# Performance work log

Hardware: AMD Instinct MI355X
Metric: run time of the kernel (lower is better)

The kernel has to match this reference:

```python
import jax, jax.numpy as jnp
import numpy as np

N_EMBD = 1024
N_HEADS = 16
HEAD_DIM = N_EMBD // N_HEADS  # 64
NUM_BUCKETS = 32
MAX_DISTANCE = 64


def _relative_position_bucket(relative_position):
    # bidirectional=False path from the torch source
    rp = jnp.maximum(-relative_position, 0)  # valid (non-positive) rel positions -> distance
    max_exact = NUM_BUCKETS // 2
    is_small = rp < max_exact
    rp_f = jnp.maximum(rp, 1).astype(jnp.float32)  # guard log(0); masked by where
    large = max_exact + (
        jnp.log(rp_f / max_exact) / np.log(MAX_DISTANCE / max_exact) * (NUM_BUCKETS - max_exact)
    ).astype(jnp.int32)
    large = jnp.minimum(large, NUM_BUCKETS - 1)
    return jnp.where(is_small, rp, large)


def setup_inputs() -> dict:
    key = jax.random.key(0)
    ks = jax.random.split(key, 10)
    B, S = 2, 2048
    std = 1.0 / np.sqrt(N_EMBD)
    inp = {
        "hidden_states": jax.random.normal(ks[0], (B, S, N_EMBD), dtype=jnp.float32),
        "Wq": jax.random.normal(ks[1], (N_EMBD, N_EMBD), dtype=jnp.float32) * std,
        "bq": jnp.zeros((N_EMBD,), jnp.float32),
        "Wk": jax.random.normal(ks[2], (N_EMBD, N_EMBD), dtype=jnp.float32) * std,
        "bk": jnp.zeros((N_EMBD,), jnp.float32),
        "Wv": jax.random.normal(ks[3], (N_EMBD, N_EMBD), dtype=jnp.float32) * std,
        "bv": jnp.zeros((N_EMBD,), jnp.float32),
        "Wo": jax.random.normal(ks[4], (N_EMBD, N_EMBD), dtype=jnp.float32) * std,
        "bo": jnp.zeros((N_EMBD,), jnp.float32),
        "rel_bias": jax.random.normal(ks[5], (NUM_BUCKETS, N_HEADS), dtype=jnp.float32) * 0.1,
    }
    return inp


def reference(hidden_states, Wq, bq, Wk, bk, Wv, bv, Wo, bo, rel_bias):
    B, S, _ = hidden_states.shape

    def shape(x):  # [B,S,E] -> [B,H,S,D]
        return x.reshape(B, S, N_HEADS, HEAD_DIM).transpose(0, 2, 1, 3)

    scale = 1.0 / np.sqrt(HEAD_DIM)
    q = shape(hidden_states @ Wq + bq)
    k = shape(hidden_states @ Wk + bk)
    v = shape(hidden_states @ Wv + bv)

    scores = jnp.einsum("bhqd,bhkd->bhqk", q * scale, k)

    ctx = jnp.arange(S)[:, None]
    mem = jnp.arange(S)[None, :]
    bucket = _relative_position_bucket(mem - ctx)  # [S,S] int
    # [S,S,H] -> [1,H,S,S]
    position_bias = rel_bias[bucket].transpose(2, 0, 1)[None]
    scores = scores + position_bias * 8.0  # note the *8 from the source

    attn = jax.nn.softmax(scores.astype(jnp.float32), axis=-1).astype(scores.dtype)
    ctx_out = jnp.einsum("bhqk,bhkd->bhqd", attn, v)
    ctx_out = ctx_out.transpose(0, 2, 1, 3).reshape(B, S, N_EMBD)
    return ctx_out @ Wo + bo
```

## Files before the change

### kernel.cpp

```cpp
#include <hip/hip_runtime.h>
#include <math.h>


#define SEQ 2048
#define EMB 1024
#define NH 16
#define HD 64
#define LOG2E 1.44269504088896340736f
#define MU (1u << 20)

typedef short v8s __attribute__((ext_vector_type(8)));
typedef float v4f __attribute__((ext_vector_type(4)));
typedef float v16f __attribute__((ext_vector_type(16)));
typedef unsigned int v4u __attribute__((ext_vector_type(4)));

__device__ __forceinline__ v4f mfma16(v8s a, v8s b, v4f c) {
  return __builtin_amdgcn_mfma_f32_16x16x32_bf16(a, b, c, 0, 0, 0);
}
__device__ __forceinline__ v16f mfma32(v8s a, v8s b, v16f c) {
  return __builtin_amdgcn_mfma_f32_32x32x16_bf16(a, b, c, 0, 0, 0);
}
__device__ __forceinline__ unsigned short bfh(float x) {
  unsigned u = __builtin_bit_cast(unsigned, x);
  return (unsigned short)((u + 0x7FFFu + ((u >> 16) & 1u)) >> 16);
}
__device__ __forceinline__ float bff(unsigned short h) {
  unsigned u = (unsigned)h << 16;
  return __builtin_bit_cast(float, u);
}
__device__ __forceinline__ int imin(int a, int b) { return a < b ? a : b; }
__device__ __forceinline__ unsigned pk2(float a, float b) {
  unsigned h;
  asm("v_cvt_pk_bf16_f32 %0, %1, %2" : "=v"(h) : "v"(a), "v"(b));
  return h;
}
__device__ __forceinline__ void split2(float a, float b, unsigned& uh, unsigned& ul) {
  const unsigned h = pk2(a, b);
  const float ra = __builtin_bit_cast(float, h << 16);
  const float rb = __builtin_bit_cast(float, h & 0xFFFF0000u);
  uh = h;
  ul = pk2(a - ra, b - rb);
}
typedef const __attribute__((address_space(1))) unsigned char* gp_t;
typedef __attribute__((address_space(3))) unsigned char* lp_t;
__device__ __forceinline__ void gload16(const void* g, void* l) {
  __builtin_amdgcn_global_load_lds((gp_t)g, (lp_t)l, 16, 0, 0);
}

__global__ __launch_bounds__(256) void prep_kernel(
    const float* __restrict__ hs, const float* __restrict__ Wq,
    const float* __restrict__ Wk, const float* __restrict__ Wv,
    const float* __restrict__ Wo, unsigned short* __restrict__ wsu) {
  __shared__ float T[64][68];
  const int t = threadIdx.x;
  const int z = blockIdx.z;
  if (z == 4) {
    unsigned short* ah = wsu + 32u * MU;
    const int base = (blockIdx.y * 16 + blockIdx.x) * 16384 + t * 4;
#pragma unroll
    for (int i = 0; i < 16; ++i) {
      const int idx = base + i * 1024;
      const float4 v = *(const float4*)(hs + idx);
      *(uint2*)&ah[idx] = make_uint2(pk2(v.x, v.y), pk2(v.z, v.w));
    }
    return;
  }
  const float* W = (z == 0) ? Wq : (z == 1) ? Wk : (z == 2) ? Wv : Wo;
  const float s = (z == 0) ? 0.125f * LOG2E : 1.0f;
  unsigned short* WTh = wsu + (size_t)(40u + 2u * z) * MU;
  unsigned short* WTl = WTh + MU;
  const int n0 = blockIdx.x * 64, k0 = blockIdx.y * 64;
  const int r = t >> 2, cs = (t & 3) * 16;
#pragma unroll
  for (int i = 0; i < 4; ++i)
    *(float4*)&T[r][cs + i * 4] =
        *(const float4*)(W + (size_t)(k0 + r) * EMB + n0 + cs + i * 4);
  __syncthreads();
  unsigned short hb[16], lb[16];
#pragma unroll
  for (int i = 0; i < 16; i += 2) {
    unsigned uh, ul;
    split2(T[cs + i][r] * s, T[cs + i + 1][r] * s, uh, ul);
    hb[i] = (unsigned short)(uh & 0xFFFFu);
    hb[i + 1] = (unsigned short)(uh >> 16);
    lb[i] = (unsigned short)(ul & 0xFFFFu);
    lb[i + 1] = (unsigned short)(ul >> 16);
  }
  const size_t go = (size_t)(n0 + r) * EMB + k0 + cs;
  *(v8s*)&WTh[go] = *(v8s*)&hb[0];
  *(v8s*)&WTh[go + 8] = *(v8s*)&hb[8];
  *(v8s*)&WTl[go] = *(v8s*)&lb[0];
  *(v8s*)&WTl[go + 8] = *(v8s*)&lb[8];
}

struct alignas(16) G2Smem {
  unsigned short Ah[128][32], Bh[128][32], Bl[128][32];
};

__device__ __forceinline__ void gemm128_2p(
    const unsigned short* __restrict__ Ah_g,
    const unsigned short* __restrict__ Bh_g,
    const unsigned short* __restrict__ Bl_g,
    int m0, int n0, G2Smem& S, v4f acc[4][4]) {
  const int t = threadIdx.x;
  const int l = t & 63, w = t >> 6;
  const int wm = (w >> 1) << 6, wn = (w & 1) << 6;
  const int lg = l >> 4, lc = l & 15;
  const int r0 = t >> 2;
  const int gl = (t & 3) ^ ((r0 >> 1) & 3);
  unsigned short* lba = &S.Ah[0][0] + w * 512;
  unsigned short* lbb = &S.Bh[0][0] + w * 512;
  unsigned short* lbl = &S.Bl[0][0] + w * 512;
  for (int k0 = 0; k0 < EMB; k0 += 32) {
    __syncthreads();
    {
      const size_t sa0 = (size_t)(m0 + r0) * EMB + k0 + gl * 8;
      const size_t sb0 = (size_t)(n0 + r0) * EMB + k0 + gl * 8;
      gload16(Ah_g + sa0, lba);
      gload16(Ah_g + sa0 + (size_t)64 * EMB, lba + 2048);
      gload16(Bh_g + sb0, lbb);
      gload16(Bh_g + sb0 + (size_t)64 * EMB, lbb + 2048);
      gload16(Bl_g + sb0, lbl);
      gload16(Bl_g + sb0 + (size_t)64 * EMB, lbl + 2048);
    }
    asm volatile("s_waitcnt vmcnt(0)" ::: "memory");
    __syncthreads();
    v8s ah[4], bh[4], bl[4];
#pragma unroll
    for (int r = 0; r < 4; ++r) {
      const int ra = wm + r * 16 + lc;
      ah[r] = *(const v8s*)&S.Ah[ra][(lg ^ ((ra >> 1) & 3)) * 8];
      const int rb = wn + r * 16 + lc;
      bh[r] = *(const v8s*)&S.Bh[rb][(lg ^ ((rb >> 1) & 3)) * 8];
      bl[r] = *(const v8s*)&S.Bl[rb][(lg ^ ((rb >> 1) & 3)) * 8];
    }
#pragma unroll
    for (int i = 0; i < 4; ++i)
#pragma unroll
      for (int j = 0; j < 4; ++j) {
        acc[i][j] = mfma16(ah[i], bh[j], acc[i][j]);
        acc[i][j] = mfma16(ah[i], bl[j], acc[i][j]);
      }
  }
  __syncthreads();
}

__global__ __launch_bounds__(256) void qkv_mfma(
    const float* __restrict__ bq, const float* __restrict__ bk,
    const float* __restrict__ bv, unsigned short* __restrict__ wsu) {
  __shared__ G2Smem S;
  const int mat = blockIdx.y >> 3;
  const int m0 = blockIdx.x << 7, n0 = (blockIdx.y & 7) << 7;
  const unsigned short* Ah_g = wsu + 32u * MU;
  const unsigned short* Bh_g = wsu + (size_t)(40u + 2u * mat) * MU;
  const unsigned short* Bl_g = Bh_g + MU;
  const float* bias = (mat == 0) ? bq : (mat == 1) ? bk : bv;
  const float bs = (mat == 0) ? 0.125f * LOG2E : 1.0f;
  unsigned short* oh = wsu + (size_t)mat * 8u * MU;
  unsigned short* ol = oh + 4u * MU;

  v4f acc[4][4] = {};
  gemm128_2p(Ah_g, Bh_g, Bl_g, m0, n0, S, acc);

  const int t = threadIdx.x, l = t & 63, w = t >> 6;
  const int wm = (w >> 1) << 6, wn = (w & 1) << 6, lg = l >> 4, lc = l & 15;
  if (mat == 0) {
#pragma unroll
    for (int i = 0; i < 4; ++i)
#pragma unroll
      for (int j = 0; j < 4; ++j)
#pragma unroll
        for (int jr = 0; jr < 4; ++jr) {
          const int r = m0 + wm + i * 16 + lg * 4 + jr;
          const int cm = n0 + wn + j * 16 + lc;
          const float val = acc[i][j][jr] + bias[cm] * bs;
          const unsigned short h = bfh(val);
          const size_t idx = (((size_t)((r >> 11) * NH + (cm >> 6)) * SEQ) +
                              (r & 2047)) * HD + (cm & 63);
          oh[idx] = h;
          ol[idx] = bfh(val - bff(h));
        }
  } else if (mat == 1) {
#pragma unroll
    for (int i = 0; i < 4; ++i)
#pragma unroll
      for (int j = 0; j < 4; ++j)
#pragma unroll
        for (int jr = 0; jr < 4; ++jr) {
          const int r = m0 + wm + i * 16 + lg * 4 + jr;
          const int cm = n0 + wn + j * 16 + lc;
          const float val = acc[i][j][jr] + bias[cm];
          const int s = r & 2047, d = cm & 63;
          const size_t idx = (((size_t)((r >> 11) * NH + (cm >> 6)) * SEQ) + s) * HD +
                             ((((d >> 3) ^ (s & 7)) << 3) | (d & 7));
          oh[idx] = bfh(val);
        }
  } else {
    unsigned short* Traw = &S.Ah[0][0];
    unsigned short (*Th)[136] = (unsigned short(*)[136])Traw;
    unsigned short (*Tl)[136] = (unsigned short(*)[136])(Traw + 32 * 136);
    const int b = m0 >> 11;
    const int s0base = m0 & 2047;
#pragma unroll
    for (int j = 0; j < 4; ++j) {
      __syncthreads();
#pragma unroll
      for (int i = 0; i < 4; ++i)
#pragma unroll
        for (int jr = 0; jr < 4; ++jr) {
          const int cm = n0 + wn + j * 16 + lc;
          const float val = acc[i][j][jr] + bias[cm];
          const unsigned short hi = bfh(val);
          const int trow = (wn >> 2) + lc;
          const int tcol = wm + i * 16 + lg * 4 + jr;
          Th[trow][tcol] = hi;
          Tl[trow][tcol] = bfh(val - bff(hi));
        }
      __syncthreads();
      const int tr = t >> 3, sgc = (t & 7) * 16;
      const int c = n0 + (tr >> 4) * 64 + j * 16 + (tr & 15);
      const int h2 = c >> 6, d = c & 63;
      const int sabs = s0base + sgc;
      const int g0 = (sabs >> 3) & 7;
      const size_t ob = ((size_t)(b * NH + h2) * HD + d) * SEQ + (sabs & ~63);
      const int o0 = (g0 ^ (d & 7)) << 3, o1 = ((g0 + 1) ^ (d & 7)) << 3;
      *(v8s*)&oh[ob + o0] = *(const v8s*)&Th[tr][sgc];
      *(v8s*)&oh[ob + o1] = *(const v8s*)&Th[tr][sgc + 8];
      *(v8s*)&ol[ob + o0] = *(const v8s*)&Tl[tr][sgc];
      *(v8s*)&ol[ob + o1] = *(const v8s*)&Tl[tr][sgc + 8];
    }
  }
}

__device__ __forceinline__ v8s pfrag(unsigned a0, unsigned a1, unsigned a2,
                                     unsigned a3, int h5) {
  const unsigned sa = (unsigned)__shfl_xor((int)(h5 ? a0 : a2), 32, 64);
  const unsigned sb = (unsigned)__shfl_xor((int)(h5 ? a1 : a3), 32, 64);
  v4u r;
  r[0] = h5 ? sa : a0;
  r[1] = h5 ? sb : a1;
  r[2] = h5 ? a2 : sa;
  r[3] = h5 ? a3 : sb;
  return __builtin_bit_cast(v8s, r);
}

__global__ __launch_bounds__(256, 3) void attn_mfma(
    const float* __restrict__ rel_bias, unsigned short* __restrict__ wsu) {
  __shared__ struct alignas(16) {
    unsigned short Kh[2][64][64];
    unsigned short VTh[2][64][64];
    unsigned short VTl[2][64][64];
    float bias8[32];
  } S;
  const int t = threadIdx.x;
  const int nid = (blockIdx.x & 7) * 128 + (blockIdx.x >> 3);
  const int half = nid >> 9;
  const int bh = (nid >> 4) & 31;
  const int qt = nid & 15;
  const int hh = bh & 15, b = bh >> 4;
  const int w = t >> 6, l = t & 63;
  const int lq = l & 31, h5 = l >> 5;
  const int qbase = qt * 128 + w * 32;
  const int kvbase = half << 10;

  const unsigned short* qh = wsu;
  const unsigned short* ql = wsu + 4u * MU;
  const unsigned short* kh = wsu + 8u * MU;
  const unsigned short* vth = wsu + 16u * MU;
  const unsigned short* vtl = wsu + 20u * MU;
  unsigned short* od = wsu + (half ? 28u : 24u) * MU;
  float2* stats = (float2*)(wsu + 36u * MU);

  if (t < 32) S.bias8[t] = rel_bias[t * NH + hh] * 8.0f * LOG2E;

  v8s qfh[4], qfl[4];
  const size_t qg = ((size_t)bh * SEQ + qbase + lq) * HD;
#pragma unroll
  for (int dc = 0; dc < 4; ++dc) {
    qfh[dc] = *(const v8s*)(qh + qg + dc * 16 + h5 * 8);
    qfl[dc] = *(const v8s*)(ql + qg + dc * 16 + h5 * 8);
  }

  float m_run = -1e30f, l_run = 0.0f;
  v16f acc[2] = {};

  const int srow = t >> 3, sg = t & 7;
  const size_t kbase_g = ((size_t)bh * SEQ + kvbase) * HD;
  const size_t vbase_g = (size_t)bh * HD * SEQ + kvbase;

  auto stage = [&](int kt, int bufsel) {
    const int kv0 = kt * 64;
    unsigned short* lk = &S.Kh[bufsel][0][0] + w * 512;
    unsigned short* lvh = &S.VTh[bufsel][0][0] + w * 512;
    unsigned short* lvl = &S.VTl[bufsel][0][0] + w * 512;
    gload16(kh + kbase_g + (size_t)(kv0 + srow) * HD + sg * 8, lk);
    gload16(kh + kbase_g + (size_t)(kv0 + srow + 32) * HD + sg * 8, lk + 2048);
    gload16(vth + vbase_g + (size_t)srow * SEQ + kv0 + sg * 8, lvh);
    gload16(vth + vbase_g + (size_t)(srow + 32) * SEQ + kv0 + sg * 8, lvh + 2048);
    gload16(vtl + vbase_g + (size_t)srow * SEQ + kv0 + sg * 8, lvl);
    gload16(vtl + vbase_g + (size_t)(srow + 32) * SEQ + kv0 + sg * 8, lvl + 2048);
  };

  stage(0, 0);
  for (int kt = 0; kt < 16; ++kt) {
    const int buf = kt & 1;
    const int kv0 = kvbase + kt * 64;
    asm volatile("s_waitcnt vmcnt(0)" ::: "memory");
    __syncthreads();
    if (kt < 15) stage(kt + 1, buf ^ 1);

    v16f sc[2] = {};
    __builtin_amdgcn_s_setprio(1);
#pragma unroll
    for (int kb = 0; kb < 2; ++kb)
#pragma unroll
      for (int dc = 0; dc < 4; ++dc) {
        const int cswz = (((dc << 1) + h5) ^ (lq & 7)) << 3;
        const v8s kfh = *(const v8s*)&S.Kh[buf][kb * 32 + lq][cswz];
        sc[kb] = mfma32(kfh, qfh[dc], sc[kb]);
        sc[kb] = mfma32(kfh, qfl[dc], sc[kb]);
      }
    __builtin_amdgcn_s_setprio(0);

#pragma unroll
    for (int kb = 0; kb < 2; ++kb) {
      const int dq = qbase - (kv0 + kb * 32);
      if (dq + 31 <= 0) {
        const float bb = S.bias8[0];
#pragma unroll
        for (int r = 0; r < 16; ++r) sc[kb][r] += bb;
      } else if (dq >= 90) {
        const float bb = S.bias8[31];
#pragma unroll
        for (int r = 0; r < 16; ++r) sc[kb][r] += bb;
      } else {
#pragma unroll
        for (int r = 0; r < 16; ++r) {
          const int krow = (r & 3) + 8 * (r >> 2) + 4 * h5;
          int rp = (qbase + lq) - (kv0 + kb * 32 + krow);
          rp = rp > 0 ? rp : 0;
          const int bu =
              rp < 16 ? rp
                      : imin(16 + (int)(8.0f * __log2f((float)rp * 0.0625f)), 31);
          sc[kb][r] += S.bias8[bu];
        }
      }
    }

    float mt = sc[0][0];
#pragma unroll
    for (int r = 1; r < 16; ++r) mt = fmaxf(mt, sc[0][r]);
#pragma unroll
    for (int r = 0; r < 16; ++r) mt = fmaxf(mt, sc[1][r]);
    mt = fmaxf(mt, __shfl_xor(mt, 32, 64));
    if (__all(mt <= m_run + 8.0f) == 0) {
      const float mn = fmaxf(m_run, mt);
      const float fac = exp2f(m_run - mn);
      l_run *= fac;
#pragma unroll
      for (int r = 0; r < 16; ++r) {
        acc[0][r] *= fac;
        acc[1][r] *= fac;
      }
      m_run = mn;
    }
    unsigned pk[16];
    float rs = 0.0f;
#pragma unroll
    for (int i = 0; i < 16; ++i) {
      const float p0 = exp2f(sc[i >> 3][(2 * i) & 15] - m_run);
      const float p1 = exp2f(sc[i >> 3][(2 * i + 1) & 15] - m_run);
      rs += p0 + p1;
      pk[i] = pk2(p0, p1);
    }
    rs += __shfl_xor(rs, 32, 64);
    l_run += rs;

    __builtin_amdgcn_s_setprio(1);
#pragma unroll
    for (int ks = 0; ks < 4; ++ks) {
      const v8s pb = pfrag(pk[4 * ks], pk[4 * ks + 1], pk[4 * ks + 2],
                           pk[4 * ks + 3], h5);
      const int cswz = (((ks << 1) + h5) ^ (lq & 7)) << 3;
#pragma unroll
      for (int db = 0; db < 2; ++db) {
        const v8s vfh = *(const v8s*)&S.VTh[buf][db * 32 + lq][cswz];
        const v8s vfl = *(const v8s*)&S.VTl[buf][db * 32 + lq][cswz];
        acc[db] = mfma32(vfh, pb, acc[db]);
        acc[db] = mfma32(vfl, pb, acc[db]);
      }
    }
    __builtin_amdgcn_s_setprio(0);
  }

  const float inv = 1.0f / l_run;
  const size_t rowb = ((size_t)b * SEQ + qbase + lq) * EMB + hh * HD;
#pragma unroll
  for (int db = 0; db < 2; ++db)
#pragma unroll
    for (int i = 0; i < 8; ++i) {
      const unsigned u = pk2(acc[db][2 * i] * inv, acc[db][2 * i + 1] * inv);
      const int d0 = db * 32 + 8 * (i >> 1) + 4 * h5 + 2 * (i & 1);
      *(unsigned*)&od[rowb + d0] = u;
    }
  if (h5 == 0)
    stats[(size_t)((half << 5) + bh) * SEQ + qbase + lq] =
        make_float2(m_run, l_run);
}

__global__ __launch_bounds__(256) void merge_kernel(unsigned short* __restrict__ wsu) {
  const int t = threadIdx.x;
  const size_t idx = ((size_t)blockIdx.x * 256 + t) * 16;
  const int row = (int)(idx >> 10);
  const int col = (int)(idx & 1023);
  const int b = row >> 11, s = row & 2047;
  const int bh = b * NH + (col >> 6);
  const float2* st = (const float2*)(wsu + 36u * MU);
  const float2 s0 = st[(size_t)bh * SEQ + s];
  const float2 s1 = st[(size_t)32 * SEQ + (size_t)bh * SEQ + s];
  const float M = fmaxf(s0.x, s1.x);
  const float w0 = s0.y * exp2f(s0.x - M);
  const float w1 = s1.y * exp2f(s1.x - M);
  const float inv = 1.0f / (w0 + w1);
  const float a0 = w0 * inv, a1 = w1 * inv;
  unsigned short* p0 = wsu + 24u * MU + idx;
  const unsigned short* p1 = wsu + 28u * MU + idx;
  const v8s x0a = *(const v8s*)p0, x0b = *(const v8s*)(p0 + 8);
  const v8s x1a = *(const v8s*)p1, x1b = *(const v8s*)(p1 + 8);
  unsigned short o[16];
#pragma unroll
  for (int e = 0; e < 8; ++e) {
    o[e] = bfh(a0 * bff((unsigned short)x0a[e]) + a1 * bff((unsigned short)x1a[e]));
    o[8 + e] =
        bfh(a0 * bff((unsigned short)x0b[e]) + a1 * bff((unsigned short)x1b[e]));
  }
  *(v8s*)p0 = *(const v8s*)&o[0];
  *(v8s*)(p0 + 8) = *(const v8s*)&o[8];
}

__global__ __launch_bounds__(256) void out_mfma(
    const float* __restrict__ bo, float* __restrict__ out,
    unsigned short* __restrict__ wsu) {
  __shared__ G2Smem S;
  const int m0 = blockIdx.x << 7, n0 = blockIdx.y << 7;
  const unsigned short* Ah_g = wsu + 24u * MU;
  const unsigned short* Bh_g = wsu + 46u * MU;
  const unsigned short* Bl_g = wsu + 47u * MU;
  v4f acc[4][4] = {};
  gemm128_2p(Ah_g, Bh_g, Bl_g, m0, n0, S, acc);
  const int t = threadIdx.x, l = t & 63, w = t >> 6;
  const int wm = (w >> 1) << 6, wn = (w & 1) << 6, lg = l >> 4, lc = l & 15;
#pragma unroll
  for (int i = 0; i < 4; ++i)
#pragma unroll
    for (int j = 0; j < 4; ++j)
#pragma unroll
      for (int jr = 0; jr < 4; ++jr) {
        const int r = m0 + wm + i * 16 + lg * 4 + jr;
        const int c = n0 + wn + j * 16 + lc;
        out[(size_t)r * EMB + c] = acc[i][j][jr] + bo[c];
      }
}

extern "C" void kernel_launch(void* const* d_in, const int* in_sizes, int n_in,
                              void* d_out, int out_size, void* d_ws, size_t ws_size,
                              hipStream_t stream) {
  const float* hs = (const float*)d_in[0];
  const float* Wq = (const float*)d_in[1];
  const float* bq = (const float*)d_in[2];
  const float* Wk = (const float*)d_in[3];
  const float* bk = (const float*)d_in[4];
  const float* Wv = (const float*)d_in[5];
  const float* bv = (const float*)d_in[6];
  const float* Wo = (const float*)d_in[7];
  const float* bo = (const float*)d_in[8];
  const float* rb = (const float*)d_in[9];
  unsigned short* wsu = (unsigned short*)d_ws;

  hipLaunchKernelGGL(prep_kernel, dim3(16, 16, 5), dim3(256), 0, stream,
                     hs, Wq, Wk, Wv, Wo, wsu);
  hipLaunchKernelGGL(qkv_mfma, dim3(32, 24), dim3(256), 0, stream, bq, bk, bv, wsu);
  hipLaunchKernelGGL(attn_mfma, dim3(1024), dim3(256), 0, stream, rb, wsu);
  hipLaunchKernelGGL(merge_kernel, dim3(1024), dim3(256), 0, stream, wsu);
  hipLaunchKernelGGL(out_mfma, dim3(32, 8), dim3(256), 0, stream, bo, (float*)d_out, wsu);
}
```

Baseline: 298.6 us.

## Drop low-order bf16 split for K and V paths, change LDS swizzle key

Stops producing and consuming the low-part bf16 correction for Wk, Wv and the V tensor. The K/V projections and the PV matmul now use a single bf16 MFMA instead of two, and less data is loaded into LDS. The freed LDS allows the attention kernel's launch bounds to target 4 blocks per CU instead of 3. The K/V swizzle key is also changed to a new skey function to reduce LDS bank conflicts. In exchange, precision drops on the K/V and PV paths, which may push error past tolerance.

```diff
diff --git a/kernel.cpp b/kernel.cpp
--- a/kernel.cpp
+++ b/kernel.cpp
@@ -45,6 +45,9 @@
 typedef __attribute__((address_space(3))) unsigned char* lp_t;
 __device__ __forceinline__ void gload16(const void* g, void* l) {
   __builtin_amdgcn_global_load_lds((gp_t)g, (lp_t)l, 16, 0, 0);
+}
+__device__ __forceinline__ int skey(int x) {
+  return ((x & 7) + ((x >> 3) & 3)) & 7;
 }
 
 __global__ __launch_bounds__(256) void prep_kernel(
@@ -67,6 +70,7 @@
   }
   const float* W = (z == 0) ? Wq : (z == 1) ? Wk : (z == 2) ? Wv : Wo;
   const float s = (z == 0) ? 0.125f * LOG2E : 1.0f;
+  const bool wlo = (z == 0 || z == 3);
   unsigned short* WTh = wsu + (size_t)(40u + 2u * z) * MU;
   unsigned short* WTl = WTh + MU;
   const int n0 = blockIdx.x * 64, k0 = blockIdx.y * 64;
@@ -79,8 +83,10 @@
   unsigned short hb[16], lb[16];
 #pragma unroll
   for (int i = 0; i < 16; i += 2) {
-    unsigned uh, ul;
-    split2(T[cs + i][r] * s, T[cs + i + 1][r] * s, uh, ul);
+    const float a = T[cs + i][r] * s, b2 = T[cs + i + 1][r] * s;
+    unsigned uh, ul = 0;
+    if (wlo) split2(a, b2, uh, ul);
+    else uh = pk2(a, b2);
     hb[i] = (unsigned short)(uh & 0xFFFFu);
     hb[i + 1] = (unsigned short)(uh >> 16);
     lb[i] = (unsigned short)(ul & 0xFFFFu);
@@ -89,19 +95,21 @@
   const size_t go = (size_t)(n0 + r) * EMB + k0 + cs;
   *(v8s*)&WTh[go] = *(v8s*)&hb[0];
   *(v8s*)&WTh[go + 8] = *(v8s*)&hb[8];
-  *(v8s*)&WTl[go] = *(v8s*)&lb[0];
-  *(v8s*)&WTl[go + 8] = *(v8s*)&lb[8];
+  if (wlo) {
+    *(v8s*)&WTl[go] = *(v8s*)&lb[0];
+    *(v8s*)&WTl[go + 8] = *(v8s*)&lb[8];
+  }
 }
 
 struct alignas(16) G2Smem {
   unsigned short Ah[128][32], Bh[128][32], Bl[128][32];
 };
 
-__device__ __forceinline__ void gemm128_2p(
+__device__ __forceinline__ void gemm128_bf(
     const unsigned short* __restrict__ Ah_g,
     const unsigned short* __restrict__ Bh_g,
     const unsigned short* __restrict__ Bl_g,
-    int m0, int n0, G2Smem& S, v4f acc[4][4]) {
+    int m0, int n0, G2Smem& S, v4f acc[4][4], const bool useBl) {
   const int t = threadIdx.x;
   const int l = t & 63, w = t >> 6;
   const int wm = (w >> 1) << 6, wn = (w & 1) << 6;
@@ -120,8 +128,10 @@
       gload16(Ah_g + sa0 + (size_t)64 * EMB, lba + 2048);
       gload16(Bh_g + sb0, lbb);
       gload16(Bh_g + sb0 + (size_t)64 * EMB, lbb + 2048);
-      gload16(Bl_g + sb0, lbl);
-      gload16(Bl_g + sb0 + (size_t)64 * EMB, lbl + 2048);
+      if (useBl) {
+        gload16(Bl_g + sb0, lbl);
+        gload16(Bl_g + sb0 + (size_t)64 * EMB, lbl + 2048);
+      }
     }
     asm volatile("s_waitcnt vmcnt(0)" ::: "memory");
     __syncthreads();
@@ -132,14 +142,14 @@
       ah[r] = *(const v8s*)&S.Ah[ra][(lg ^ ((ra >> 1) & 3)) * 8];
       const int rb = wn + r * 16 + lc;
       bh[r] = *(const v8s*)&S.Bh[rb][(lg ^ ((rb >> 1) & 3)) * 8];
-      bl[r] = *(const v8s*)&S.Bl[rb][(lg ^ ((rb >> 1) & 3)) * 8];
+      if (useBl) bl[r] = *(const v8s*)&S.Bl[rb][(lg ^ ((rb >> 1) & 3)) * 8];
     }
 #pragma unroll
     for (int i = 0; i < 4; ++i)
 #pragma unroll
       for (int j = 0; j < 4; ++j) {
         acc[i][j] = mfma16(ah[i], bh[j], acc[i][j]);
-        acc[i][j] = mfma16(ah[i], bl[j], acc[i][j]);
+        if (useBl) acc[i][j] = mfma16(ah[i], bl[j], acc[i][j]);
       }
   }
   __syncthreads();
@@ -155,12 +165,11 @@
   const unsigned short* Bh_g = wsu + (size_t)(40u + 2u * mat) * MU;
   const unsigned short* Bl_g = Bh_g + MU;
   const float* bias = (mat == 0) ? bq : (mat == 1) ? bk : bv;
-  const float bs = (mat == 0) ? 0.125f * LOG2E : 1.0f;
   unsigned short* oh = wsu + (size_t)mat * 8u * MU;
   unsigned short* ol = oh + 4u * MU;
 
   v4f acc[4][4] = {};
-  gemm128_2p(Ah_g, Bh_g, Bl_g, m0, n0, S, acc);
+  gemm128_bf(Ah_g, Bh_g, Bl_g, m0, n0, S, acc, mat == 0);
 
   const int t = threadIdx.x, l = t & 63, w = t >> 6;
   const int wm = (w >> 1) << 6, wn = (w & 1) << 6, lg = l >> 4, lc = l & 15;
@@ -173,7 +182,7 @@
         for (int jr = 0; jr < 4; ++jr) {
           const int r = m0 + wm + i * 16 + lg * 4 + jr;
           const int cm = n0 + wn + j * 16 + lc;
-          const float val = acc[i][j][jr] + bias[cm] * bs;
+          const float val = acc[i][j][jr] + bias[cm] * (0.125f * LOG2E);
           const unsigned short h = bfh(val);
           const size_t idx = (((size_t)((r >> 11) * NH + (cm >> 6)) * SEQ) +
                               (r & 2047)) * HD + (cm & 63);
@@ -192,13 +201,12 @@
           const float val = acc[i][j][jr] + bias[cm];
           const int s = r & 2047, d = cm & 63;
           const size_t idx = (((size_t)((r >> 11) * NH + (cm >> 6)) * SEQ) + s) * HD +
-                             ((((d >> 3) ^ (s & 7)) << 3) | (d & 7));
+                             ((((d >> 3) ^ skey(s)) << 3) | (d & 7));
           oh[idx] = bfh(val);
         }
   } else {
     unsigned short* Traw = &S.Ah[0][0];
     unsigned short (*Th)[136] = (unsigned short(*)[136])Traw;
-    unsigned short (*Tl)[136] = (unsigned short(*)[136])(Traw + 32 * 136);
     const int b = m0 >> 11;
     const int s0base = m0 & 2047;
 #pragma unroll
@@ -210,11 +218,9 @@
         for (int jr = 0; jr < 4; ++jr) {
           const int cm = n0 + wn + j * 16 + lc;
           const float val = acc[i][j][jr] + bias[cm];
-          const unsigned short hi = bfh(val);
           const int trow = (wn >> 2) + lc;
           const int tcol = wm + i * 16 + lg * 4 + jr;
-          Th[trow][tcol] = hi;
-          Tl[trow][tcol] = bfh(val - bff(hi));
+          Th[trow][tcol] = bfh(val);
         }
       __syncthreads();
       const int tr = t >> 3, sgc = (t & 7) * 16;
@@ -223,11 +229,9 @@
       const int sabs = s0base + sgc;
       const int g0 = (sabs >> 3) & 7;
       const size_t ob = ((size_t)(b * NH + h2) * HD + d) * SEQ + (sabs & ~63);
-      const int o0 = (g0 ^ (d & 7)) << 3, o1 = ((g0 + 1) ^ (d & 7)) << 3;
+      const int o0 = (g0 ^ skey(d)) << 3, o1 = ((g0 + 1) ^ skey(d)) << 3;
       *(v8s*)&oh[ob + o0] = *(const v8s*)&Th[tr][sgc];
       *(v8s*)&oh[ob + o1] = *(const v8s*)&Th[tr][sgc + 8];
-      *(v8s*)&ol[ob + o0] = *(const v8s*)&Tl[tr][sgc];
-      *(v8s*)&ol[ob + o1] = *(const v8s*)&Tl[tr][sgc + 8];
     }
   }
 }
@@ -244,12 +248,11 @@
   return __builtin_bit_cast(v8s, r);
 }
 
-__global__ __launch_bounds__(256, 3) void attn_mfma(
+__global__ __launch_bounds__(256, 4) void attn_mfma(
     const float* __restrict__ rel_bias, unsigned short* __restrict__ wsu) {
   __shared__ struct alignas(16) {
     unsigned short Kh[2][64][64];
     unsigned short VTh[2][64][64];
-    unsigned short VTl[2][64][64];
     float bias8[32];
   } S;
   const int t = threadIdx.x;
@@ -262,12 +265,12 @@
   const int lq = l & 31, h5 = l >> 5;
   const int qbase = qt * 128 + w * 32;
   const int kvbase = half << 10;
+  const int kkey = skey(lq);
 
   const unsigned short* qh = wsu;
   const unsigned short* ql = wsu + 4u * MU;
   const unsigned short* kh = wsu + 8u * MU;
   const unsigned short* vth = wsu + 16u * MU;
-  const unsigned short* vtl = wsu + 20u * MU;
   unsigned short* od = wsu + (half ? 28u : 24u) * MU;
   float2* stats = (float2*)(wsu + 36u * MU);
 
@@ -292,13 +295,10 @@
     const int kv0 = kt * 64;
     unsigned short* lk = &S.Kh[bufsel][0][0] + w * 512;
     unsigned short* lvh = &S.VTh[bufsel][0][0] + w * 512;
-    unsigned short* lvl = &S.VTl[bufsel][0][0] + w * 512;
     gload16(kh + kbase_g + (size_t)(kv0 + srow) * HD + sg * 8, lk);
     gload16(kh + kbase_g + (size_t)(kv0 + srow + 32) * HD + sg * 8, lk + 2048);
     gload16(vth + vbase_g + (size_t)srow * SEQ + kv0 + sg * 8, lvh);
     gload16(vth + vbase_g + (size_t)(srow + 32) * SEQ + kv0 + sg * 8, lvh + 2048);
-    gload16(vtl + vbase_g + (size_t)srow * SEQ + kv0 + sg * 8, lvl);
-    gload16(vtl + vbase_g + (size_t)(srow + 32) * SEQ + kv0 + sg * 8, lvl + 2048);
   };
 
   stage(0, 0);
@@ -315,7 +315,7 @@
     for (int kb = 0; kb < 2; ++kb)
 #pragma unroll
       for (int dc = 0; dc < 4; ++dc) {
-        const int cswz = (((dc << 1) + h5) ^ (lq & 7)) << 3;
+        const int cswz = (((dc << 1) + h5) ^ kkey) << 3;
         const v8s kfh = *(const v8s*)&S.Kh[buf][kb * 32 + lq][cswz];
         sc[kb] = mfma32(kfh, qfh[dc], sc[kb]);
         sc[kb] = mfma32(kfh, qfl[dc], sc[kb]);
@@ -381,13 +381,11 @@
     for (int ks = 0; ks < 4; ++ks) {
       const v8s pb = pfrag(pk[4 * ks], pk[4 * ks + 1], pk[4 * ks + 2],
                            pk[4 * ks + 3], h5);
-      const int cswz = (((ks << 1) + h5) ^ (lq & 7)) << 3;
+      const int vswz = (((ks << 1) + h5) ^ kkey) << 3;
 #pragma unroll
       for (int db = 0; db < 2; ++db) {
-        const v8s vfh = *(const v8s*)&S.VTh[buf][db * 32 + lq][cswz];
-        const v8s vfl = *(const v8s*)&S.VTl[buf][db * 32 + lq][cswz];
+        const v8s vfh = *(const v8s*)&S.VTh[buf][db * 32 + lq][vswz];
         acc[db] = mfma32(vfh, pb, acc[db]);
-        acc[db] = mfma32(vfl, pb, acc[db]);
       }
     }
     __builtin_amdgcn_s_setprio(0);
@@ -447,7 +445,7 @@
   const unsigned short* Bh_g = wsu + 46u * MU;
   const unsigned short* Bl_g = wsu + 47u * MU;
   v4f acc[4][4] = {};
-  gemm128_2p(Ah_g, Bh_g, Bl_g, m0, n0, S, acc);
+  gemm128_bf(Ah_g, Bh_g, Bl_g, m0, n0, S, acc, true);
   const int t = threadIdx.x, l = t & 63, w = t >> 6;
   const int wm = (w >> 1) << 6, wn = (w & 1) << 6, lg = l >> 4, lc = l & 15;
 #pragma unroll
```

New measurement: 306.1 us. +2.5%, slower.
